# Performance work log

Hardware: AMD Instinct MI355X
Metric: run time of the kernel (lower is better)

## Reference

```python
import jax, jax.numpy as jnp
import numpy as np

N_CH = 62
F_DIM = 16
T_DIM = 32
B_DIM = 256
N_NODES = B_DIM * N_CH  # 15872
E_DIM = 200000
SEQ = T_DIM * F_DIM  # 512


def setup_inputs() -> dict:
    key = jax.random.key(0)
    ks = iter(jax.random.split(key, 40))
    s = 0.05
    inp = {}
    inp['x'] = jax.random.normal(next(ks), (N_NODES, F_DIM, T_DIM), dtype=jnp.float32)
    inp['edge_index'] = jax.random.randint(next(ks), (T_DIM, 2, E_DIM), 0, N_NODES, dtype=jnp.int64)
    inp['edge_weight'] = jax.random.uniform(next(ks), (T_DIM, E_DIM), dtype=jnp.float32)
    inp['batch'] = jax.random.randint(next(ks), (T_DIM, N_NODES), 0, B_DIM, dtype=jnp.int64)
    # ChebConv params (K=2): lins have no bias, single bias added at end
    for p in ['c1', 'c2']:
        inp[p + '_w0'] = jax.random.normal(next(ks), (F_DIM, F_DIM), dtype=jnp.float32) * s
        inp[p + '_w1'] = jax.random.normal(next(ks), (F_DIM, F_DIM), dtype=jnp.float32) * s
        inp[p + '_b'] = jnp.zeros((F_DIM,), jnp.float32)
    # LSTM params (torch gate order i,f,g,o); fold b_ih+b_hh into one bias
    for name, i_dim, h_dim in [('l1', N_CH, 64), ('l2', 64, 128), ('l3', 128, 256)]:
        inp[name + '_wih'] = jax.random.normal(next(ks), (4 * h_dim, i_dim), dtype=jnp.float32) * s
        inp[name + '_whh'] = jax.random.normal(next(ks), (4 * h_dim, h_dim), dtype=jnp.float32) * s
        inp[name + '_b'] = jnp.zeros((4 * h_dim,), jnp.float32)
    # MLP head
    for name, i_dim, o_dim in [('fc1', SEQ * 256, 256), ('fc2', 256, 128), ('fc3', 128, 64), ('fc4', 64, 4)]:
        inp[name + '_w'] = jax.random.normal(next(ks), (i_dim, o_dim), dtype=jnp.float32) * s
        inp[name + '_b'] = jnp.zeros((o_dim,), jnp.float32)
    return inp


def _cheb(x, src, dst, w, w0, w1, b):
    # PyG ChebConv K=2, sym norm, lambda_max=2: Tx1 = -D^{-1/2} A D^{-1/2} x
    n = x.shape[0]
    deg = jax.ops.segment_sum(w, src, num_segments=n)
    dinv = jnp.where(deg > 0, jax.lax.rsqrt(deg), 0.0)
    norm = -dinv[src] * w * dinv[dst]
    tx1 = jax.ops.segment_sum(norm[:, None] * x[src], dst, num_segments=n)
    return x @ w0 + tx1 @ w1 + b


def _lstm(x, wih, whh, b):
    # x: [B, S, I] -> [B, S, H], batch_first, zero init state
    bsz, _, _ = x.shape
    h_dim = whh.shape[1]
    xg = x @ wih.T + b  # precompute input gates [B, S, 4H]
    def step(carry, xt):
        h, c = carry
        g = xt + h @ whh.T
        i, f, gg, o = jnp.split(g, 4, axis=-1)
        c = jax.nn.sigmoid(f) * c + jax.nn.sigmoid(i) * jnp.tanh(gg)
        h = jax.nn.sigmoid(o) * jnp.tanh(c)
        return (h, c), h
    h0 = jnp.zeros((bsz, h_dim), x.dtype)
    _, hs = jax.lax.scan(step, (h0, h0), jnp.swapaxes(xg, 0, 1))
    return jnp.swapaxes(hs, 0, 1)


def reference(x, edge_index, edge_weight, batch,
              c1_w0, c1_w1, c1_b, c2_w0, c2_w1, c2_b,
              l1_wih, l1_whh, l1_b, l2_wih, l2_whh, l2_b, l3_wih, l3_whh, l3_b,
              fc1_w, fc1_b, fc2_w, fc2_b, fc3_w, fc3_b, fc4_w, fc4_b):
    def per_t(xt, ei, w):
        h = _cheb(xt, ei[0], ei[1], w, c1_w0, c1_w1, c1_b)
        h = jax.nn.leaky_relu(h, 0.01)
        return _cheb(h, ei[0], ei[1], w, c2_w0, c2_w1, c2_b)
    xt_first = jnp.moveaxis(x, -1, 0)  # [T, N, F]
    h = jax.vmap(per_t)(xt_first, edge_index, edge_weight)  # [T, N, F]
    xc = jnp.moveaxis(h, 0, -1)  # [N, F, T]
    xc = xc.reshape(B_DIM, N_CH, F_DIM, T_DIM)
    xc = jnp.transpose(xc, (0, 3, 2, 1))  # [B, T, F, 62]
    xc = xc.reshape(B_DIM, T_DIM * F_DIM, N_CH)  # [B, S, 62]
    h = _lstm(xc, l1_wih, l1_whh, l1_b)
    h = _lstm(h, l2_wih, l2_whh, l2_b)
    h = _lstm(h, l3_wih, l3_whh, l3_b)
    z = h.reshape(B_DIM, -1)  # [B, S*256]
    z = jax.nn.relu(z @ fc1_w + fc1_b)
    z = jax.nn.relu(z @ fc2_w + fc2_b)
    z = jax.nn.relu(z @ fc3_w + fc3_b)
    return z @ fc4_w + fc4_b
```

## Files before the change

### kernel.cpp

```cpp
#include <hip/hip_runtime.h>
#include <cstdint>
#include <cstddef>


#define T_DIM 32
#define F_DIMC 16
#define NNODE 15872
#define EDGES 200000
#define BATCH 256
#define SEQL 512
#define TN (T_DIM * NNODE)
#define TE (T_DIM * EDGES)
#define ESEG 25000
#define NWORK 208

typedef unsigned short ushortT;
typedef __bf16 bf16_t;
typedef bf16_t bf16x8 __attribute__((ext_vector_type(8)));
typedef float f32x4 __attribute__((ext_vector_type(4)));

__device__ __forceinline__ ushortT f2bf(float f) {
  union { float f; unsigned u; } v; v.f = f;
  unsigned u = v.u;
  u += 0x7fffu + ((u >> 16) & 1u);
  return (ushortT)(u >> 16);
}
__device__ __forceinline__ float fsig(float x) { return 1.0f / (1.0f + __expf(-x)); }
__device__ __forceinline__ float ftanh(float x) {
  float e = __expf(2.0f * x);
  return 1.0f - 2.0f / (e + 1.0f);
}
#define PIN(v) asm volatile("" : "+v"(v))

__device__ __forceinline__ void bar_sync() {
  asm volatile("s_waitcnt lgkmcnt(0)\n\ts_barrier" ::: "memory");
  __builtin_amdgcn_sched_barrier(0);
}

__device__ __forceinline__ uint32_t aload(const uint32_t* p) {
  return __hip_atomic_load(p, __ATOMIC_RELAXED, __HIP_MEMORY_SCOPE_AGENT);
}
__device__ __forceinline__ void astore(uint32_t* p, uint32_t v) {
  __hip_atomic_store(p, v, __ATOMIC_RELAXED, __HIP_MEMORY_SCOPE_AGENT);
}

__global__ void k_wprep(const float* __restrict__ w1i, const float* __restrict__ w1h,
                        const float* __restrict__ w2i, const float* __restrict__ w2h,
                        const float* __restrict__ w3i, const float* __restrict__ w3h,
                        ushortT* __restrict__ Wcat) {
  int id = blockIdx.x * 256 + threadIdx.x;
  if (id >= 524288) return;
  float v;
  if (id < 32768) {
    int g = id >> 7, k = id & 127;
    v = (k < 62) ? w1i[g * 62 + k] : ((k >= 64) ? w1h[g * 64 + (k - 64)] : 0.0f);
  } else if (id < 131072) {
    int j = id - 32768; int g = j / 192, k = j % 192;
    v = (k < 64) ? w2i[g * 64 + k] : w2h[g * 128 + (k - 64)];
  } else {
    int j = id - 131072; int g = j / 384, k = j % 384;
    v = (k < 128) ? w3i[g * 128 + k] : w3h[g * 256 + (k - 128)];
  }
  Wcat[id] = f2bf(v);
}

__global__ void k_transpose(const float* __restrict__ x, float* __restrict__ xt) {
  __shared__ float s[528];
  int n = blockIdx.x;
  int tid = threadIdx.x;
  for (int i = tid; i < 512; i += 256) {
    s[(i >> 5) * 33 + (i & 31)] = x[(size_t)n * 512 + i];
  }
  __syncthreads();
  for (int i = tid; i < 512; i += 256) {
    int t = i >> 4, f = i & 15;
    xt[((size_t)t * NNODE + n) * 16 + f] = s[f * 33 + t];
  }
}

__global__ __launch_bounds__(1024, 1) void k_hist8(const int* __restrict__ ei,
                                                   const float* __restrict__ ew,
                                                   float* __restrict__ pdeg,
                                                   int* __restrict__ pcnt,
                                                   int* __restrict__ rank) {
  __shared__ float sdeg[NNODE];
  __shared__ int scnt[NNODE];
  int t = blockIdx.x >> 3;
  int b = blockIdx.x & 7;
  int tid = threadIdx.x;
  for (int i = tid; i < NNODE; i += 1024) { sdeg[i] = 0.0f; scnt[i] = 0; }
  __syncthreads();
  const int* srcp = ei + (size_t)(2 * t) * EDGES;
  const int* dstp = ei + (size_t)(2 * t + 1) * EDGES;
  const float* ewp = ew + (size_t)t * EDGES;
  int* rankp = rank + (size_t)t * EDGES;
  int e0 = b * ESEG, e1 = e0 + ESEG;
  for (int e = e0 + tid; e < e1; e += 1024) {
    int src = srcp[e];
    int dst = dstp[e];
    float w = ewp[e];
    atomicAdd(&sdeg[src], w);
    rankp[e] = atomicAdd(&scnt[dst], 1);
  }
  __syncthreads();
  float* pd = pdeg + (size_t)blockIdx.x * NNODE;
  int* pc = pcnt + (size_t)blockIdx.x * NNODE;
  for (int i = tid; i < NNODE; i += 1024) {
    pd[i] = sdeg[i];
    pc[i] = scnt[i];
  }
}

__global__ void k_mergescan(const float* __restrict__ pdeg,
                            const int* __restrict__ pcnt,
                            int* __restrict__ offs, int* __restrict__ ctot,
                            float* __restrict__ dinv, int* __restrict__ bko) {
  __shared__ int s[256];
  int tid = threadIdx.x;
  int gid = blockIdx.x * 256 + tid;
  int t = gid / NNODE, n = gid % NNODE;
  int base = t * 8;
  float d = 0.0f;
  int v = 0;
  int pref[8];
#pragma unroll
  for (int b = 0; b < 8; ++b) {
    pref[b] = v;
    d += pdeg[(size_t)(base + b) * NNODE + n];
    v += pcnt[(size_t)(base + b) * NNODE + n];
  }
#pragma unroll
  for (int b = 0; b < 8; ++b) bko[(size_t)gid * 8 + b] = pref[b];
  dinv[gid] = (d > 0.0f) ? rsqrtf(d) : 0.0f;
  s[tid] = v; __syncthreads();
  for (int off = 1; off < 256; off <<= 1) {
    int x = (tid >= off) ? s[tid - off] : 0;
    __syncthreads();
    s[tid] += x;
    __syncthreads();
  }
  offs[gid] = s[tid] - v;
  if (tid == 255) ctot[blockIdx.x] = s[255];
}

__global__ void k_scanB(const int* __restrict__ ctot, int* __restrict__ cbase) {
  __shared__ int s[256];
  int tid = threadIdx.x;
  int carry = 0;
  for (int c = 0; c < 8; ++c) {
    int i = c * 256 + tid;
    int v = (i < 1984) ? ctot[i] : 0;
    s[tid] = v; __syncthreads();
    for (int off = 1; off < 256; off <<= 1) {
      int x = (tid >= off) ? s[tid - off] : 0;
      __syncthreads();
      s[tid] += x;
      __syncthreads();
    }
    if (i < 1984) cbase[i] = carry + s[tid] - v;
    int tot = s[255];
    __syncthreads();
    carry += tot;
  }
}

__global__ void k_fill2(const int* __restrict__ ei, const float* __restrict__ ew,
                        const float* __restrict__ dinv, const int* __restrict__ offs,
                        const int* __restrict__ cbase, const int* __restrict__ bko,
                        const int* __restrict__ rank,
                        int* __restrict__ csrs, float* __restrict__ csrn) {
  int id = blockIdx.x * 256 + threadIdx.x;
  if (id >= TE) return;
  int t = id / EDGES, e = id % EDGES;
  int src = ei[(size_t)(2 * t) * EDGES + e];
  int dst = ei[(size_t)(2 * t + 1) * EDGES + e];
  int idx = t * NNODE + dst;
  int seg = e / ESEG;
  int pos = offs[idx] + cbase[idx >> 8] + bko[(size_t)idx * 8 + seg] + rank[id];
  csrs[pos] = src;
  csrn[pos] = -dinv[t * NNODE + src] * ew[id] * dinv[idx];
}

__device__ __forceinline__ void fma4(float4& a, float sc, const float4 b) {
  a.x += sc * b.x; a.y += sc * b.y; a.z += sc * b.z; a.w += sc * b.w;
}

__global__ void k_gc1(const float* __restrict__ in, const int* __restrict__ offs,
                      const int* __restrict__ cbase,
                      const int* __restrict__ csrs, const float* __restrict__ csrn,
                      const float* __restrict__ w0, const float* __restrict__ w1,
                      const float* __restrict__ bias, float* __restrict__ outF) {
  __shared__ float sw0[256], sw1[256], sb[16];
  int tid = threadIdx.x;
  sw0[tid] = w0[tid];
  sw1[tid] = w1[tid];
  if (tid < 16) sb[tid] = bias[tid];
  __syncthreads();
  int idx = blockIdx.x * 256 + tid;
  if (idx >= TN) return;
  int t = idx / NNODE;
  const float4* rowp = (const float4*)(in + (size_t)idx * 16);
  float4 x0 = rowp[0], x1 = rowp[1], x2 = rowp[2], x3 = rowp[3];
  float4 a0 = {0, 0, 0, 0}, a1 = {0, 0, 0, 0}, a2 = {0, 0, 0, 0}, a3 = {0, 0, 0, 0};
  int beg = offs[idx] + cbase[idx >> 8];
  int end = (idx == TN - 1) ? TE : offs[idx + 1] + cbase[(idx + 1) >> 8];
  const float* base = in + (size_t)t * NNODE * 16;
  for (int p2 = beg; p2 < end; ++p2) {
    int s = csrs[p2];
    float nr = csrn[p2];
    const float4* rp = (const float4*)(base + (size_t)s * 16);
    fma4(a0, nr, rp[0]); fma4(a1, nr, rp[1]); fma4(a2, nr, rp[2]); fma4(a3, nr, rp[3]);
  }
  float xr[16], ar[16];
  *(float4*)&xr[0] = x0; *(float4*)&xr[4] = x1; *(float4*)&xr[8] = x2; *(float4*)&xr[12] = x3;
  *(float4*)&ar[0] = a0; *(float4*)&ar[4] = a1; *(float4*)&ar[8] = a2; *(float4*)&ar[12] = a3;
  float o[16];
#pragma unroll
  for (int j = 0; j < 16; ++j) o[j] = sb[j];
#pragma unroll
  for (int k = 0; k < 16; ++k) {
    float xv = xr[k], av = ar[k];
#pragma unroll
    for (int j = 0; j < 16; ++j) o[j] += xv * sw0[k * 16 + j] + av * sw1[k * 16 + j];
  }
#pragma unroll
  for (int j = 0; j < 16; ++j) o[j] = (o[j] > 0.0f) ? o[j] : 0.01f * o[j];
  float4* op = (float4*)(outF + (size_t)idx * 16);
  op[0] = *(float4*)&o[0]; op[1] = *(float4*)&o[4];
  op[2] = *(float4*)&o[8]; op[3] = *(float4*)&o[12];
}

__global__ __launch_bounds__(512, 1) void k_mega(
    const uint32_t* __restrict__ xc32_c, uint32_t* __restrict__ xc32,
    const ushortT* __restrict__ Wcat,
    const float* __restrict__ b1g, const float* __restrict__ b2g,
    const float* __restrict__ b3g,
    ushortT* __restrict__ zbuf, uint32_t* __restrict__ h2x,
    uint32_t* __restrict__ xbuf,
    const float* __restrict__ h1buf, const int* __restrict__ offs,
    const int* __restrict__ cbase, const int* __restrict__ csrs,
    const float* __restrict__ csrn,
    const float* __restrict__ c2w0, const float* __restrict__ c2w1,
    const float* __restrict__ c2b) {
  __shared__ ushortT X1[2][16 * 72];
  __shared__ ushortT H1[2][16 * 72];
  __shared__ ushortT H2[2][16 * 136];
  __shared__ ushortT HS[2][16 * 136];
  __shared__ ushortT PS[2][16 * 136];
  __shared__ ushortT H2S[2][16 * 136];
  __shared__ float swa[256], swb[256], sbb[16];
  int tid = threadIdx.x;
  int wv = tid >> 6, lane = tid & 63;
  int col = lane & 15, koff = (lane >> 4) * 8, m = lane & 15;
  int bx = blockIdx.x;

  if (bx >= 48) {
    if (tid < 256) { swa[tid] = c2w0[tid]; swb[tid] = c2w1[tid]; }
    if (tid < 16) sbb[tid] = c2b[tid];
    __syncthreads();
    int wtid = (bx - 48) * 512 + tid;
    for (int t = 0; t < 32; ++t) {
      uint32_t tag = ((uint32_t)(t + 1)) << 16;
      const float* h1t = h1buf + (size_t)t * NNODE * 16;
      const int* csrsp = csrs;
      const float* csrnp = csrn;
      for (int n = wtid; n < NNODE; n += NWORK * 512) {
        int idx = t * NNODE + n;
        int beg = offs[idx] + cbase[idx >> 8];
        int end = (idx == TN - 1) ? TE : offs[idx + 1] + cbase[(idx + 1) >> 8];
        const float4* rowp = (const float4*)(h1t + (size_t)n * 16);
        float4 x0 = rowp[0], x1 = rowp[1], x2 = rowp[2], x3 = rowp[3];
        float4 a0 = {0, 0, 0, 0}, a1 = {0, 0, 0, 0}, a2 = {0, 0, 0, 0}, a3 = {0, 0, 0, 0};
        const float* basei = h1buf + (size_t)t * NNODE * 16;
        for (int p2 = beg; p2 < end; ++p2) {
          int s = csrsp[p2];
          float nr = csrnp[p2];
          const float4* rp = (const float4*)(basei + (size_t)s * 16);
          fma4(a0, nr, rp[0]); fma4(a1, nr, rp[1]); fma4(a2, nr, rp[2]); fma4(a3, nr, rp[3]);
        }
        float xr[16], ar[16];
        *(float4*)&xr[0] = x0; *(float4*)&xr[4] = x1; *(float4*)&xr[8] = x2; *(float4*)&xr[12] = x3;
        *(float4*)&ar[0] = a0; *(float4*)&ar[4] = a1; *(float4*)&ar[8] = a2; *(float4*)&ar[12] = a3;
        float o[16];
#pragma unroll
        for (int j = 0; j < 16; ++j) o[j] = sbb[j];
#pragma unroll
        for (int k = 0; k < 16; ++k) {
          float xv = xr[k], av = ar[k];
#pragma unroll
          for (int j = 0; j < 16; ++j) o[j] += xv * swa[k * 16 + j] + av * swb[k * 16 + j];
        }
        int bb = n / 62, ch = n % 62;
#pragma unroll
        for (int j = 0; j < 16; ++j)
          astore(&xc32[((size_t)(bb * 512 + t * 16 + j)) * 64 + ch], tag | f2bf(o[j]));
        if (ch < 2) {
#pragma unroll
          for (int j = 0; j < 16; ++j)
            astore(&xc32[((size_t)(bb * 512 + t * 16 + j)) * 64 + 62 + ch], tag);
        }
      }
    }
    return;
  }

  if (bx < 16) {
    int g = bx;
    int bg = g * 16;
    const ushortT* W1 = Wcat;
    const ushortT* W2 = Wcat + 32768;

    bf16x8 w1r[4][4];
    if (wv < 4) {
#pragma unroll
      for (int q = 0; q < 4; ++q)
#pragma unroll
        for (int k = 0; k < 4; ++k) {
          w1r[q][k] = *reinterpret_cast<const bf16x8*>(
              &W1[(size_t)(q * 64 + wv * 16 + col) * 128 + k * 32 + koff]);
          PIN(w1r[q][k]);
        }
    }
    bf16x8 w2r[4][6];
#pragma unroll
    for (int q = 0; q < 4; ++q)
#pragma unroll
      for (int k = 0; k < 6; ++k) {
        w2r[q][k] = *reinterpret_cast<const bf16x8*>(
            &W2[(size_t)(q * 128 + wv * 16 + col) * 192 + k * 32 + koff]);
        PIN(w2r[q][k]);
      }
    float b1v[4] = {0, 0, 0, 0}, b2v[4];
    if (wv < 4) {
#pragma unroll
      for (int q = 0; q < 4; ++q) b1v[q] = b1g[q * 64 + wv * 16 + col];
    }
#pragma unroll
    for (int q = 0; q < 4; ++q) b2v[q] = b2g[q * 128 + wv * 16 + col];

    float c1r[4] = {0, 0, 0, 0};
    float c2r[4] = {0, 0, 0, 0};

    for (int i = tid; i < 2 * 16 * 72; i += 512) { X1[0][i] = 0; H1[0][i] = 0; }
    for (int i = tid; i < 2 * 16 * 136; i += 512) H2[0][i] = 0;
    __syncthreads();
    uint4 xreg = {0, 0, 0, 0};
    {
      int tid2 = tid - 256;
      if (tid2 >= 0 && tid2 < 128) {
        int mm = tid2 >> 3, jj = (tid2 & 7) * 8;
        const uint32_t* p0 = &xc32_c[((size_t)(bg + mm) * 512 + 0) * 64 + jj];
        uint32_t w[8];
#pragma unroll
        for (int i = 0; i < 8; ++i) w[i] = aload(p0 + i);
        for (;;) {
          bool ok = true;
#pragma unroll
          for (int i = 0; i < 8; ++i)
            if ((w[i] >> 16) != 1u) { ok = false; w[i] = aload(p0 + i); }
          if (ok) break;
        }
        uint4 v;
        v.x = (w[0] & 0xffffu) | (w[1] << 16);
        v.y = (w[2] & 0xffffu) | (w[3] << 16);
        v.z = (w[4] & 0xffffu) | (w[5] << 16);
        v.w = (w[6] & 0xffffu) | (w[7] << 16);
        *(uint4*)&X1[0][mm * 72 + jj] = v;
        const uint32_t* p1 = &xc32_c[((size_t)(bg + mm) * 512 + 1) * 64 + jj];
#pragma unroll
        for (int i = 0; i < 8; ++i) w[i] = aload(p1 + i);
        for (;;) {
          bool ok = true;
#pragma unroll
          for (int i = 0; i < 8; ++i)
            if ((w[i] >> 16) != 1u) { ok = false; w[i] = aload(p1 + i); }
          if (ok) break;
        }
        xreg.x = (w[0] & 0xffffu) | (w[1] << 16);
        xreg.y = (w[2] & 0xffffu) | (w[3] << 16);
        xreg.z = (w[4] & 0xffffu) | (w[5] << 16);
        xreg.w = (w[6] & 0xffffu) | (w[7] << 16);
      }
    }
    __syncthreads();

    uint32_t* h2g = h2x + (size_t)g * 512 * 2048;

    for (int t = 0; t < 512; ++t) {
      int pr = t & 1, pw = 1 - pr;
      if (wv < 4) {
        f32x4 acc[4] = {};
#pragma unroll
        for (int kt = 0; kt < 4; ++kt) {
          const ushortT* ap = (kt < 2) ? &X1[pr][m * 72 + kt * 32 + koff]
                                       : &H1[pr][m * 72 + (kt - 2) * 32 + koff];
          bf16x8 a = *reinterpret_cast<const bf16x8*>(ap);
#pragma unroll
          for (int q = 0; q < 4; ++q)
            acc[q] = __builtin_amdgcn_mfma_f32_16x16x32_bf16(a, w1r[q][kt], acc[q], 0, 0, 0);
        }
#pragma unroll
        for (int r = 0; r < 4; ++r) {
          int row = (lane >> 4) * 4 + r;
          int lc = wv * 16 + col;
          float gi = acc[0][r] + b1v[0];
          float gf = acc[1][r] + b1v[1];
          float gg = acc[2][r] + b1v[2];
          float go = acc[3][r] + b1v[3];
          float c = fsig(gf) * c1r[r] + fsig(gi) * ftanh(gg);
          float h = fsig(go) * ftanh(c);
          c1r[r] = c;
          H1[pw][row * 72 + lc] = f2bf(h);
        }
      } else {
        int tid2 = tid - 256;
        if (tid2 < 128) {
          int mm = tid2 >> 3, jj = (tid2 & 7) * 8;
          if (t + 1 < 512)
            *(uint4*)&X1[pw][mm * 72 + jj] = xreg;
          int tf = (t + 2 < 512) ? t + 2 : 511;
          const uint32_t* pp = &xc32_c[((size_t)(bg + mm) * 512 + tf) * 64 + jj];
          uint32_t want = (uint32_t)((tf >> 4) + 1);
          uint32_t w[8];
#pragma unroll
          for (int i = 0; i < 8; ++i) w[i] = aload(pp + i);
          for (;;) {
            bool ok = true;
#pragma unroll
            for (int i = 0; i < 8; ++i)
              if ((w[i] >> 16) != want) { ok = false; w[i] = aload(pp + i); }
            if (ok) break;
          }
          xreg.x = (w[0] & 0xffffu) | (w[1] << 16);
          xreg.y = (w[2] & 0xffffu) | (w[3] << 16);
          xreg.z = (w[4] & 0xffffu) | (w[5] << 16);
          xreg.w = (w[6] & 0xffffu) | (w[7] << 16);
        }
      }
      bar_sync();
      {
        f32x4 acc[4] = {};
#pragma unroll
        for (int kt = 0; kt < 6; ++kt) {
          const ushortT* ap = (kt < 2) ? &H1[pw][m * 72 + kt * 32 + koff]
                                       : &H2[pr][m * 136 + (kt - 2) * 32 + koff];
          bf16x8 a = *reinterpret_cast<const bf16x8*>(ap);
#pragma unroll
          for (int q = 0; q < 4; ++q)
            acc[q] = __builtin_amdgcn_mfma_f32_16x16x32_bf16(a, w2r[q][kt], acc[q], 0, 0, 0);
        }
        uint32_t tag = ((uint32_t)(t + 1)) << 16;
#pragma unroll
        for (int r = 0; r < 4; ++r) {
          int row = (lane >> 4) * 4 + r;
          int lc = wv * 16 + col;
          float gi = acc[0][r] + b2v[0];
          float gf = acc[1][r] + b2v[1];
          float gg = acc[2][r] + b2v[2];
          float go = acc[3][r] + b2v[3];
          float c = fsig(gf) * c2r[r] + fsig(gi) * ftanh(gg);
          float h = fsig(go) * ftanh(c);
          c2r[r] = c;
          ushortT hb = f2bf(h);
          H2[pw][row * 136 + lc] = hb;
          astore(&h2g[(size_t)t * 2048 + row * 128 + lc], tag | hb);
        }
      }
      bar_sync();
    }
  } else {
    int bxx = bx - 16;
    int s = (bxx >> 3) & 1;
    int g = (bxx & 7) | ((bxx >> 4) << 3);
    int ps = 1 - s;
    int bg = g * 16;
    const ushortT* W3 = Wcat + 131072;

    bf16x8 wH[4][4], wO[4][4], wP[4][4];
#pragma unroll
    for (int q = 0; q < 4; ++q) {
      const ushortT* rw = &W3[(size_t)(q * 256 + s * 128 + wv * 16 + col) * 384];
#pragma unroll
      for (int j = 0; j < 4; ++j) {
        wH[q][j] = *reinterpret_cast<const bf16x8*>(&rw[j * 32 + koff]);
        wO[q][j] = *reinterpret_cast<const bf16x8*>(&rw[(4 + s * 4 + j) * 32 + koff]);
        wP[q][j] = *reinterpret_cast<const bf16x8*>(&rw[(4 + ps * 4 + j) * 32 + koff]);
        PIN(wH[q][j]); PIN(wO[q][j]); PIN(wP[q][j]);
      }
    }
    float b3v[4];
#pragma unroll
    for (int q = 0; q < 4; ++q) b3v[q] = b3g[q * 256 + s * 128 + wv * 16 + col];

    float c3r[4] = {0, 0, 0, 0};

    for (int i = tid; i < 2 * 16 * 136; i += 512) HS[0][i] = 0;
    __syncthreads();

    uint32_t* myslot = xbuf + (((size_t)g * 2 + s) * 2) * 2048;
    const uint32_t* pslot = xbuf + (((size_t)g * 2 + ps) * 2) * 2048;
    const uint32_t* h2g = h2x + (size_t)g * 512 * 2048;

    int prow = tid >> 5, pc0 = (tid & 31) * 4;

    {
      const uint32_t* hp = h2g + prow * 128 + pc0;
      uint32_t u0 = aload(hp + 0), u1 = aload(hp + 1), u2 = aload(hp + 2), u3 = aload(hp + 3);
      for (;;) {
        bool ok = ((u0 >> 16) == 1u) & ((u1 >> 16) == 1u) &
                  ((u2 >> 16) == 1u) & ((u3 >> 16) == 1u);
        if (ok) break;
        u0 = aload(hp + 0); u1 = aload(hp + 1); u2 = aload(hp + 2); u3 = aload(hp + 3);
      }
      H2S[0][prow * 136 + pc0 + 0] = (ushortT)(u0 & 0xffffu);
      H2S[0][prow * 136 + pc0 + 1] = (ushortT)(u1 & 0xffffu);
      H2S[0][prow * 136 + pc0 + 2] = (ushortT)(u2 & 0xffffu);
      H2S[0][prow * 136 + pc0 + 3] = (ushortT)(u3 & 0xffffu);
    }
    __syncthreads();

    for (int t = 0; t < 512; ++t) {
      int prt = t & 1, pw = 1 - prt;
      const uint32_t* pb = pslot + (size_t)prt * 2048 + prow * 128 + pc0;
      uint32_t v0 = 0, v1 = 0, v2 = 0, v3 = 0;
      if (t > 0) {
        v0 = aload(pb + 0); v1 = aload(pb + 1); v2 = aload(pb + 2); v3 = aload(pb + 3);
      }
      const uint32_t* hp = h2g + (size_t)(t + 1) * 2048 + prow * 128 + pc0;
      uint32_t u0 = 0, u1 = 0, u2 = 0, u3 = 0;
      if (t < 511) {
        u0 = aload(hp + 0); u1 = aload(hp + 1); u2 = aload(hp + 2); u3 = aload(hp + 3);
      }
      __builtin_amdgcn_sched_barrier(0);
      f32x4 acc[4] = {};
#pragma unroll
      for (int kt = 0; kt < 4; ++kt) {
        bf16x8 a = *reinterpret_cast<const bf16x8*>(&H2S[prt][m * 136 + kt * 32 + koff]);
#pragma unroll
        for (int q = 0; q < 4; ++q)
          acc[q] = __builtin_amdgcn_mfma_f32_16x16x32_bf16(a, wH[q][kt], acc[q], 0, 0, 0);
      }
      if (t > 0) {
#pragma unroll
        for (int j = 0; j < 4; ++j) {
          bf16x8 a = *reinterpret_cast<const bf16x8*>(&HS[prt][m * 136 + j * 32 + koff]);
#pragma unroll
          for (int q = 0; q < 4; ++q)
            acc[q] = __builtin_amdgcn_mfma_f32_16x16x32_bf16(a, wO[q][j], acc[q], 0, 0, 0);
        }
        {
          uint32_t want = (uint32_t)t;
          while (((v0 >> 16) != want) | ((v1 >> 16) != want) |
                 ((v2 >> 16) != want) | ((v3 >> 16) != want)) {
            v0 = aload(pb + 0); v1 = aload(pb + 1); v2 = aload(pb + 2); v3 = aload(pb + 3);
          }
          PS[prt][prow * 136 + pc0 + 0] = (ushortT)(v0 & 0xffffu);
          PS[prt][prow * 136 + pc0 + 1] = (ushortT)(v1 & 0xffffu);
          PS[prt][prow * 136 + pc0 + 2] = (ushortT)(v2 & 0xffffu);
          PS[prt][prow * 136 + pc0 + 3] = (ushortT)(v3 & 0xffffu);
        }
        bar_sync();
#pragma unroll
        for (int j = 0; j < 4; ++j) {
          bf16x8 a = *reinterpret_cast<const bf16x8*>(&PS[prt][m * 136 + j * 32 + koff]);
#pragma unroll
          for (int q = 0; q < 4; ++q)
            acc[q] = __builtin_amdgcn_mfma_f32_16x16x32_bf16(a, wP[q][j], acc[q], 0, 0, 0);
        }
      }
      if (t < 511) {
        uint32_t want = (uint32_t)(t + 2);
        while (((u0 >> 16) != want) | ((u1 >> 16) != want) |
               ((u2 >> 16) != want) | ((u3 >> 16) != want)) {
          u0 = aload(hp + 0); u1 = aload(hp + 1); u2 = aload(hp + 2); u3 = aload(hp + 3);
        }
        H2S[pw][prow * 136 + pc0 + 0] = (ushortT)(u0 & 0xffffu);
        H2S[pw][prow * 136 + pc0 + 1] = (ushortT)(u1 & 0xffffu);
        H2S[pw][prow * 136 + pc0 + 2] = (ushortT)(u2 & 0xffffu);
        H2S[pw][prow * 136 + pc0 + 3] = (ushortT)(u3 & 0xffffu);
      }
      uint32_t* mw = myslot + (size_t)((t + 1) & 1) * 2048;
      ushortT hbs[4];
#pragma unroll
      for (int r = 0; r < 4; ++r) {
        int row = (lane >> 4) * 4 + r;
        int lc = wv * 16 + col;
        float gi = acc[0][r] + b3v[0];
        float gf = acc[1][r] + b3v[1];
        float gg = acc[2][r] + b3v[2];
        float go = acc[3][r] + b3v[3];
        float c = fsig(gf) * c3r[r] + fsig(gi) * ftanh(gg);
        float h = fsig(go) * ftanh(c);
        c3r[r] = c;
        hbs[r] = f2bf(h);
        astore(mw + row * 128 + lc, ((uint32_t)(t + 1) << 16) | hbs[r]);
      }
      asm volatile("s_waitcnt vmcnt(0)" ::: "memory");
      __builtin_amdgcn_sched_barrier(0);
#pragma unroll
      for (int r = 0; r < 4; ++r) {
        int row = (lane >> 4) * 4 + r;
        int lc = wv * 16 + col;
        HS[pw][row * 136 + lc] = hbs[r];
        zbuf[((size_t)(bg + row) * 512 + t) * 256 + s * 128 + lc] = hbs[r];
      }
      bar_sync();
    }
  }
}

__global__ __launch_bounds__(256) void k_fc1(const ushortT* __restrict__ zbuf,
                                             const float* __restrict__ w,
                                             float* __restrict__ part) {
  __shared__ ushortT As[256 * 40];
  __shared__ ushortT Bs[64 * 40];
  int tid = threadIdx.x;
  int kb = blockIdx.x;
  int nb = blockIdx.y;
  int wv = tid >> 6, lane = tid & 63;
  int col = lane & 15, koff = (lane >> 4) * 8;
  int k0base = kb * 2048;
  f32x4 acc[4][4] = {};
  for (int kt = 0; kt < 64; ++kt) {
    int k0 = k0base + kt * 32;
    {
      const uint4* src = (const uint4*)(zbuf + (size_t)tid * 131072 + k0);
      uint4* dst = (uint4*)(As + tid * 40);
      dst[0] = src[0]; dst[1] = src[1]; dst[2] = src[2]; dst[3] = src[3];
    }
    {
      int kk = tid >> 3, j0 = (tid & 7) * 8;
      const float* srcw = w + (size_t)(k0 + kk) * 256 + nb * 64 + j0;
#pragma unroll
      for (int jj = 0; jj < 8; ++jj) Bs[(j0 + jj) * 40 + kk] = f2bf(srcw[jj]);
    }
    __syncthreads();
    bf16x8 bfr[4];
#pragma unroll
    for (int nt = 0; nt < 4; ++nt)
      bfr[nt] = *reinterpret_cast<const bf16x8*>(&Bs[(nt * 16 + col) * 40 + koff]);
#pragma unroll
    for (int mt = 0; mt < 4; ++mt) {
      bf16x8 afr = *reinterpret_cast<const bf16x8*>(&As[(wv * 64 + mt * 16 + col) * 40 + koff]);
#pragma unroll
      for (int nt = 0; nt < 4; ++nt)
        acc[mt][nt] = __builtin_amdgcn_mfma_f32_16x16x32_bf16(afr, bfr[nt], acc[mt][nt], 0, 0, 0);
    }
    __syncthreads();
  }
#pragma unroll
  for (int mt = 0; mt < 4; ++mt)
#pragma unroll
    for (int nt = 0; nt < 4; ++nt)
#pragma unroll
      for (int r = 0; r < 4; ++r) {
        int m = wv * 64 + mt * 16 + (lane >> 4) * 4 + r;
        int n = nb * 64 + nt * 16 + col;
        part[(size_t)kb * 65536 + m * 256 + n] = acc[mt][nt][r];
      }
}

__global__ void k_fc1red(const float* __restrict__ part, const float* __restrict__ b,
                         float* __restrict__ out) {
  int id4 = blockIdx.x * 256 + threadIdx.x;
  if (id4 >= 16384) return;
  float4 s = {0.0f, 0.0f, 0.0f, 0.0f};
  for (int kb = 0; kb < 64; ++kb) {
    float4 v = *(const float4*)&part[(size_t)kb * 65536 + id4 * 4];
    s.x += v.x; s.y += v.y; s.z += v.z; s.w += v.w;
  }
  int n0 = (id4 * 4) & 255;
  s.x = fmaxf(s.x + b[n0 + 0], 0.0f);
  s.y = fmaxf(s.y + b[n0 + 1], 0.0f);
  s.z = fmaxf(s.z + b[n0 + 2], 0.0f);
  s.w = fmaxf(s.w + b[n0 + 3], 0.0f);
  *(float4*)&out[id4 * 4] = s;
}

__global__ void k_fcv(const float* __restrict__ in, const float* __restrict__ w,
                      const float* __restrict__ b, float* __restrict__ out,
                      int K, int Nn, int doRelu) {
  int id = blockIdx.x * 256 + threadIdx.x;
  int m = id / Nn, n = id % Nn;
  float s = b[n];
  for (int k = 0; k < K; ++k) s += in[m * K + k] * w[k * Nn + n];
  if (doRelu) s = fmaxf(s, 0.0f);
  out[id] = s;
}

extern "C" void kernel_launch(void* const* d_in, const int* in_sizes, int n_in,
                              void* d_out, int out_size, void* d_ws, size_t ws_size,
                              hipStream_t stream) {
  (void)in_sizes; (void)n_in; (void)out_size; (void)ws_size;
  const float* x    = (const float*)d_in[0];
  const int* ei     = (const int*)d_in[1];
  const float* ew   = (const float*)d_in[2];
  const float* c1w0 = (const float*)d_in[4];
  const float* c1w1 = (const float*)d_in[5];
  const float* c1b  = (const float*)d_in[6];
  const float* c2w0 = (const float*)d_in[7];
  const float* c2w1 = (const float*)d_in[8];
  const float* c2b  = (const float*)d_in[9];
  const float* l1wi = (const float*)d_in[10];
  const float* l1wh = (const float*)d_in[11];
  const float* l1b  = (const float*)d_in[12];
  const float* l2wi = (const float*)d_in[13];
  const float* l2wh = (const float*)d_in[14];
  const float* l2b  = (const float*)d_in[15];
  const float* l3wi = (const float*)d_in[16];
  const float* l3wh = (const float*)d_in[17];
  const float* l3b  = (const float*)d_in[18];
  const float* fc1w = (const float*)d_in[19];
  const float* fc1b = (const float*)d_in[20];
  const float* fc2w = (const float*)d_in[21];
  const float* fc2b = (const float*)d_in[22];
  const float* fc3w = (const float*)d_in[23];
  const float* fc3b = (const float*)d_in[24];
  const float* fc4w = (const float*)d_in[25];
  const float* fc4b = (const float*)d_in[26];
  float* out = (float*)d_out;

  char* p = (char*)d_ws;
  auto alloc = [&](size_t bytes) { void* r = (void*)p; p += (bytes + 255) & ~(size_t)255; return r; };
  float* xt      = (float*)alloc(32505856);
  float* h1buf   = (float*)alloc(32505856);
  float* dinv    = (float*)alloc(2031616);
  int* offs      = (int*)alloc(2031616);
  int* ctot      = (int*)alloc(8192);
  int* cbase     = (int*)alloc(8192);
  int* csrs      = (int*)alloc(25600000);
  float* csrn    = (float*)alloc(25600000);
  uint32_t* xc32 = (uint32_t*)alloc(33554432);
  ushortT* Wcat  = (ushortT*)alloc(1048576);
  ushortT* zbuf  = (ushortT*)alloc(67108864);
  float* part    = (float*)alloc(16777216);
  float* fo1     = (float*)alloc(262144);
  float* fo2     = (float*)alloc(131072);
  float* fo3     = (float*)alloc(65536);
  uint32_t* xbuf = (uint32_t*)alloc(524288);
  uint32_t* h2x  = (uint32_t*)alloc(67108864);
  int* rank = (int*)h1buf;
  float* pdeg = (float*)zbuf;
  int* pcnt = (int*)((char*)zbuf + 16777216);
  int* bko = (int*)((char*)zbuf + 35127296);


  k_wprep<<<2048, 256, 0, stream>>>(l1wi, l1wh, l2wi, l2wh, l3wi, l3wh, Wcat);
  k_transpose<<<15872, 256, 0, stream>>>(x, xt);
  k_hist8<<<256, 1024, 0, stream>>>(ei, ew, pdeg, pcnt, rank);
  k_mergescan<<<1984, 256, 0, stream>>>(pdeg, pcnt, offs, ctot, dinv, bko);
  k_scanB<<<1, 256, 0, stream>>>(ctot, cbase);
  k_fill2<<<25000, 256, 0, stream>>>(ei, ew, dinv, offs, cbase, bko, rank, csrs, csrn);
  k_gc1<<<1984, 256, 0, stream>>>(xt, offs, cbase, csrs, csrn, c1w0, c1w1, c1b, h1buf);
  k_mega<<<256, 512, 0, stream>>>(xc32, xc32, Wcat, l1b, l2b, l3b, zbuf, h2x,
                                  xbuf, h1buf, offs, cbase, csrs, csrn,
                                  c2w0, c2w1, c2b);
  k_fc1<<<dim3(64, 4), 256, 0, stream>>>(zbuf, fc1w, part);
  k_fc1red<<<64, 256, 0, stream>>>(part, fc1b, fo1);
  k_fcv<<<128, 256, 0, stream>>>(fo1, fc2w, fc2b, fo2, 256, 128, 1);
  k_fcv<<<64, 256, 0, stream>>>(fo2, fc3w, fc3b, fo3, 128, 64, 1);
  k_fcv<<<4, 256, 0, stream>>>(fo3, fc4w, fc4b, out, 64, 4, 0);
}
```

Baseline: 2.913 ms.

## Fuse fc1 GEMM into mega kernel, overlapped with LSTM via done flags

Removes the separate fc1 kernel launch. The idle worker blocks of the mega kernel now compute fc1 partial GEMM tiles as soon as each 8-timestep chunk of the LSTM output has been written, and LSTM blocks signal this through per-chunk done flags. The LSTM output stores are also packed into 32-bit pairs using lane shuffles. This aims to hide the fc1 GEMM behind the serial LSTM recurrence, at the cost of extra shared memory, spin-waiting, and a periodic vmcnt drain in the LSTM loop. The done flags carry a fixed tag with no per-call epoch, so stale flags from an earlier call could let fc1 read zbuf too early.

```diff
diff --git a/kernel.cpp b/kernel.cpp
--- a/kernel.cpp
+++ b/kernel.cpp
@@ -241,7 +241,9 @@
     const int* __restrict__ cbase, const int* __restrict__ csrs,
     const float* __restrict__ csrn,
     const float* __restrict__ c2w0, const float* __restrict__ c2w1,
-    const float* __restrict__ c2b) {
+    const float* __restrict__ c2b,
+    const float* __restrict__ fc1w, float* __restrict__ part,
+    uint32_t* __restrict__ done) {
   __shared__ ushortT X1[2][16 * 72];
   __shared__ ushortT H1[2][16 * 72];
   __shared__ ushortT H2[2][16 * 136];
@@ -249,6 +251,8 @@
   __shared__ ushortT PS[2][16 * 136];
   __shared__ ushortT H2S[2][16 * 136];
   __shared__ float swa[256], swb[256], sbb[16];
+  __shared__ ushortT fAs[256 * 40];
+  __shared__ ushortT fBs[64 * 40];
   int tid = threadIdx.x;
   int wv = tid >> 6, lane = tid & 63;
   int col = lane & 15, koff = (lane >> 4) * 8, m = lane & 15;
@@ -262,8 +266,6 @@
     for (int t = 0; t < 32; ++t) {
       uint32_t tag = ((uint32_t)(t + 1)) << 16;
       const float* h1t = h1buf + (size_t)t * NNODE * 16;
-      const int* csrsp = csrs;
-      const float* csrnp = csrn;
       for (int n = wtid; n < NNODE; n += NWORK * 512) {
         int idx = t * NNODE + n;
         int beg = offs[idx] + cbase[idx >> 8];
@@ -271,11 +273,10 @@
         const float4* rowp = (const float4*)(h1t + (size_t)n * 16);
         float4 x0 = rowp[0], x1 = rowp[1], x2 = rowp[2], x3 = rowp[3];
         float4 a0 = {0, 0, 0, 0}, a1 = {0, 0, 0, 0}, a2 = {0, 0, 0, 0}, a3 = {0, 0, 0, 0};
-        const float* basei = h1buf + (size_t)t * NNODE * 16;
         for (int p2 = beg; p2 < end; ++p2) {
-          int s = csrsp[p2];
-          float nr = csrnp[p2];
-          const float4* rp = (const float4*)(basei + (size_t)s * 16);
+          int s = csrs[p2];
+          float nr = csrn[p2];
+          const float4* rp = (const float4*)(h1t + (size_t)s * 16);
           fma4(a0, nr, rp[0]); fma4(a1, nr, rp[1]); fma4(a2, nr, rp[2]); fma4(a3, nr, rp[3]);
         }
         float xr[16], ar[16];
@@ -300,6 +301,53 @@
             astore(&xc32[((size_t)(bb * 512 + t * 16 + j)) * 64 + 62 + ch], tag);
         }
       }
+    }
+    for (int item = bx - 48; item < 256; item += NWORK) {
+      int kb = item >> 2, nb = item & 3;
+      if (tid < 32) {
+        uint32_t want = 0x5A5A0000u | (uint32_t)kb;
+        while (aload(&done[kb * 32 + tid]) != want) {}
+      }
+      __syncthreads();
+      f32x4 facc[2][4] = {};
+      int k0base = kb * 2048;
+      for (int kt2 = 0; kt2 < 64; ++kt2) {
+        int k0 = k0base + kt2 * 32;
+        {
+          const uint4* src = (const uint4*)(zbuf + (size_t)(tid >> 1) * 131072 + k0 + (tid & 1) * 16);
+          uint4* dst = (uint4*)(fAs + (tid >> 1) * 40 + (tid & 1) * 16);
+          dst[0] = src[0]; dst[1] = src[1];
+          int kk = tid >> 4, j0 = (tid & 15) * 4;
+          const float* srcw = fc1w + (size_t)(k0 + kk) * 256 + nb * 64 + j0;
+#pragma unroll
+          for (int jj = 0; jj < 4; ++jj) fBs[(j0 + jj) * 40 + kk] = f2bf(srcw[jj]);
+        }
+        __syncthreads();
+        {
+          bf16x8 bfr[4];
+#pragma unroll
+          for (int nt = 0; nt < 4; ++nt)
+            bfr[nt] = *reinterpret_cast<const bf16x8*>(&fBs[(nt * 16 + col) * 40 + koff]);
+#pragma unroll
+          for (int mt = 0; mt < 2; ++mt) {
+            bf16x8 afr = *reinterpret_cast<const bf16x8*>(&fAs[(wv * 32 + mt * 16 + col) * 40 + koff]);
+#pragma unroll
+            for (int nt = 0; nt < 4; ++nt)
+              facc[mt][nt] = __builtin_amdgcn_mfma_f32_16x16x32_bf16(afr, bfr[nt], facc[mt][nt], 0, 0, 0);
+          }
+        }
+        __syncthreads();
+      }
+#pragma unroll
+      for (int mt = 0; mt < 2; ++mt)
+#pragma unroll
+        for (int nt = 0; nt < 4; ++nt)
+#pragma unroll
+          for (int r = 0; r < 4; ++r) {
+            int mm2 = wv * 32 + mt * 16 + (lane >> 4) * 4 + r;
+            int nn2 = nb * 64 + nt * 16 + col;
+            part[(size_t)kb * 65536 + mm2 * 256 + nn2] = facc[mt][nt][r];
+          }
     }
     return;
   }
@@ -602,62 +650,22 @@
         int row = (lane >> 4) * 4 + r;
         int lc = wv * 16 + col;
         HS[pw][row * 136 + lc] = hbs[r];
-        zbuf[((size_t)(bg + row) * 512 + t) * 256 + s * 128 + lc] = hbs[r];
+        uint32_t mine = hbs[r];
+        uint32_t other = __shfl_xor(mine, 1);
+        if ((lane & 1) == 0) {
+          astore((uint32_t*)&zbuf[((size_t)(bg + row) * 512 + t) * 256 + s * 128 + lc],
+                 mine | (other << 16));
+        }
+      }
+      if ((t & 7) == 7) {
+        asm volatile("s_waitcnt vmcnt(0)" ::: "memory");
       }
       bar_sync();
-    }
-  }
-}
-
-__global__ __launch_bounds__(256) void k_fc1(const ushortT* __restrict__ zbuf,
-                                             const float* __restrict__ w,
-                                             float* __restrict__ part) {
-  __shared__ ushortT As[256 * 40];
-  __shared__ ushortT Bs[64 * 40];
-  int tid = threadIdx.x;
-  int kb = blockIdx.x;
-  int nb = blockIdx.y;
-  int wv = tid >> 6, lane = tid & 63;
-  int col = lane & 15, koff = (lane >> 4) * 8;
-  int k0base = kb * 2048;
-  f32x4 acc[4][4] = {};
-  for (int kt = 0; kt < 64; ++kt) {
-    int k0 = k0base + kt * 32;
-    {
-      const uint4* src = (const uint4*)(zbuf + (size_t)tid * 131072 + k0);
-      uint4* dst = (uint4*)(As + tid * 40);
-      dst[0] = src[0]; dst[1] = src[1]; dst[2] = src[2]; dst[3] = src[3];
-    }
-    {
-      int kk = tid >> 3, j0 = (tid & 7) * 8;
-      const float* srcw = w + (size_t)(k0 + kk) * 256 + nb * 64 + j0;
-#pragma unroll
-      for (int jj = 0; jj < 8; ++jj) Bs[(j0 + jj) * 40 + kk] = f2bf(srcw[jj]);
-    }
-    __syncthreads();
-    bf16x8 bfr[4];
-#pragma unroll
-    for (int nt = 0; nt < 4; ++nt)
-      bfr[nt] = *reinterpret_cast<const bf16x8*>(&Bs[(nt * 16 + col) * 40 + koff]);
-#pragma unroll
-    for (int mt = 0; mt < 4; ++mt) {
-      bf16x8 afr = *reinterpret_cast<const bf16x8*>(&As[(wv * 64 + mt * 16 + col) * 40 + koff]);
-#pragma unroll
-      for (int nt = 0; nt < 4; ++nt)
-        acc[mt][nt] = __builtin_amdgcn_mfma_f32_16x16x32_bf16(afr, bfr[nt], acc[mt][nt], 0, 0, 0);
-    }
-    __syncthreads();
-  }
-#pragma unroll
-  for (int mt = 0; mt < 4; ++mt)
-#pragma unroll
-    for (int nt = 0; nt < 4; ++nt)
-#pragma unroll
-      for (int r = 0; r < 4; ++r) {
-        int m = wv * 64 + mt * 16 + (lane >> 4) * 4 + r;
-        int n = nb * 64 + nt * 16 + col;
-        part[(size_t)kb * 65536 + m * 256 + n] = acc[mt][nt][r];
-      }
+      if ((t & 7) == 7 && tid == 0) {
+        astore(&done[(t >> 3) * 32 + bxx], 0x5A5A0000u | (uint32_t)(t >> 3));
+      }
+    }
+  }
 }
 
 __global__ void k_fc1red(const float* __restrict__ part, const float* __restrict__ b,
@@ -739,6 +747,7 @@
   float* fo3     = (float*)alloc(65536);
   uint32_t* xbuf = (uint32_t*)alloc(524288);
   uint32_t* h2x  = (uint32_t*)alloc(67108864);
+  uint32_t* done = (uint32_t*)alloc(8192);
   int* rank = (int*)h1buf;
   float* pdeg = (float*)zbuf;
   int* pcnt = (int*)((char*)zbuf + 16777216);
@@ -754,8 +763,7 @@
   k_gc1<<<1984, 256, 0, stream>>>(xt, offs, cbase, csrs, csrn, c1w0, c1w1, c1b, h1buf);
   k_mega<<<256, 512, 0, stream>>>(xc32, xc32, Wcat, l1b, l2b, l3b, zbuf, h2x,
                                   xbuf, h1buf, offs, cbase, csrs, csrn,
-                                  c2w0, c2w1, c2b);
-  k_fc1<<<dim3(64, 4), 256, 0, stream>>>(zbuf, fc1w, part);
+                                  c2w0, c2w1, c2b, fc1w, part, done);
   k_fc1red<<<64, 256, 0, stream>>>(part, fc1b, fo1);
   k_fcv<<<128, 256, 0, stream>>>(fo1, fc2w, fc2b, fo2, 256, 128, 1);
   k_fcv<<<64, 256, 0, stream>>>(fo2, fc3w, fc3b, fo3, 128, 64, 1);
```

Result: slower. 3.934 ms (+35.0%).
